# Kernel optimization log

Hardware: AMD Instinct MI355X
Metric: run time of the kernel (lower is better)

The kernel has to match this reference:

```python
import jax, jax.numpy as jnp
import numpy as np

H = 8            # n_heads
CLIP = 10.0      # tanh_clipping
CAPACITY = 1.0   # AgentVRP.VEHICLE_CAPACITY


def setup_inputs() -> dict:
    key = jax.random.key(0)
    ks = jax.random.split(key, 12)
    B, N, D = 256, 1000, 128
    s = 1.0 / np.sqrt(D)  # keep pre-tanh logits in a sane range
    return {
        "embeddings": jax.random.normal(ks[0], (B, N, D), jnp.float32),
        "mean_graph_emb": jax.random.normal(ks[1], (B, D), jnp.float32),
        "used_capacity": jax.random.uniform(ks[2], (B, 1), jnp.float32),
        "prev_node": jax.random.randint(ks[3], (B, 1), 0, N),
        "mask": jax.random.randint(ks[4], (B, 1, N), 0, 2).astype(bool),
        "wq_context": jax.random.normal(ks[5], (D, D), jnp.float32) * s,
        "wq_step_context": jax.random.normal(ks[6], (D + 1, D), jnp.float32) * s,
        "wk": jax.random.normal(ks[7], (D, D), jnp.float32) * s,
        "wk_tanh": jax.random.normal(ks[8], (D, D), jnp.float32) * s,
        "wv": jax.random.normal(ks[9], (D, D), jnp.float32) * s,
        "w_out": jax.random.normal(ks[10], (D, D), jnp.float32) * s,
    }


def reference(embeddings, mean_graph_emb, used_capacity, prev_node, mask,
              wq_context, wq_step_context, wk, wk_tanh, wv, w_out):
    B, N, D = embeddings.shape
    hd = D // H
    neg_inf = jnp.float32(-np.inf)

    # --- get_projections ---
    K = (embeddings @ wk).reshape(B, N, H, hd).transpose(0, 2, 1, 3)       # bhnd
    V = (embeddings @ wv).reshape(B, N, H, hd).transpose(0, 2, 1, 3)       # bhnd
    K_tanh = embeddings @ wk_tanh                                          # bnD
    Q_context = (mean_graph_emb @ wq_context)[:, None, :]                  # b1D

    # --- get_step_context ---
    cur = jnp.take_along_axis(embeddings, prev_node[:, :, None].astype(jnp.int32), axis=1)  # b1D
    step_ctx = jnp.concatenate([cur, CAPACITY - used_capacity[:, :, None]], axis=-1)        # b1(D+1)
    Q = Q_context + step_ctx @ wq_step_context                             # b1D
    Qh = Q.reshape(B, 1, H, hd).transpose(0, 2, 1, 3)                      # bh1d

    # --- decoder_mha (seq_len_q = 1) ---
    compat = jnp.einsum('bhqd,bhnd->bhqn', Qh, K) / jnp.sqrt(jnp.float32(hd))
    compat = jnp.where(mask[:, None, :, :], neg_inf, compat)
    attn = jax.nn.softmax(compat, axis=-1)
    out = jnp.einsum('bhqn,bhnd->bhqd', attn, V)
    mha = out.transpose(0, 2, 1, 3).reshape(B, 1, D) @ w_out               # b1D

    # --- get_log_p (single head, tanh-clipped) ---
    logits = jnp.einsum('bqD,bnD->bqn', mha, K_tanh) / jnp.sqrt(jnp.float32(D))
    logits = jnp.tanh(logits) * CLIP
    logits = jnp.where(mask, neg_inf, logits)
    log_p = jax.nn.log_softmax(logits, axis=-1)                            # b1n
    return log_p
```

## Files before the change

### kernel.cpp

```cpp
#include <hip/hip_runtime.h>
#include <hip/hip_bf16.h>
#include <math.h>

constexpr int kB = 256;
constexpr int kN = 1000;
constexpr int kD = 128;
constexpr int kH = 8;

#define MASK_FILL (-1.0e30f)

__device__ __forceinline__ bool is_masked(const void* m, int flag, int idx) {
  if (flag == 1) return ((const unsigned char*)m)[idx] != 0;
  if (flag == 0) return ((const int*)m)[idx] != 0;
  return ((const float*)m)[idx] != 0.0f;
}

__global__ __launch_bounds__(128) void q_kernel(
    const float* __restrict__ emb, const float* __restrict__ mge,
    const float* __restrict__ ucap, const int* __restrict__ prev,
    const float* __restrict__ wq_ctx, const float* __restrict__ wq_step,
    const float* __restrict__ wk, float* __restrict__ qt,
    const unsigned char* __restrict__ mb, int* __restrict__ flag) {
  const int b = blockIdx.x, t = threadIdx.x;
  __shared__ float cur[kD];
  __shared__ float Qs[kD];
  __shared__ int nonbin, off123;
  if (b == 0 && t == 0) { nonbin = 0; off123 = 0; }
  const float* crow = emb + ((size_t)b * kN + prev[b]) * kD;
  cur[t] = crow[t];
  __syncthreads();
  if (b == 0) {
    int l_nonbin = 0, l_off = 0;
    for (int i = t; i < 4096; i += 128) {
      unsigned char v = mb[i];
      if (v > 1) l_nonbin = 1;
      if (v != 0 && (i & 3) != 0) l_off = 1;
    }
    if (l_nonbin) atomicOr(&nonbin, 1);
    if (l_off) atomicOr(&off123, 1);
  }
  float acc = 0.f;
  const float* mger = mge + (size_t)b * kD;
  #pragma unroll 4
  for (int e = 0; e < kD; ++e) {
    acc += mger[e] * wq_ctx[e * kD + t];
    acc += cur[e] * wq_step[e * kD + t];
  }
  acc += (1.0f - ucap[b]) * wq_step[kD * kD + t];
  Qs[t] = acc;
  __syncthreads();
  if (b == 0 && t == 0) *flag = nonbin ? 2 : (off123 ? 1 : 0);
  float a8[8] = {};
  const float* wkrow = wk + (size_t)t * kD;
  #pragma unroll
  for (int h = 0; h < 8; ++h) {
    #pragma unroll
    for (int j = 0; j < 16; ++j)
      a8[h] += wkrow[h * 16 + j] * Qs[h * 16 + j];
  }
  #pragma unroll
  for (int h = 0; h < 8; ++h)
    qt[((size_t)b * 8 + h) * kD + t] = a8[h] * 0.25f;
}

__global__ __launch_bounds__(1024) void attn_stream_kernel(
    const float* __restrict__ emb, const float* __restrict__ qt_g,
    const void* __restrict__ mask, const int* __restrict__ flagp,
    float* __restrict__ pw, float* __restrict__ pl) {
  const int b = blockIdx.x, t = threadIdx.x;
  __shared__ __align__(16) float red[16][1024];
  __shared__ float lred[16][8];
  __shared__ unsigned char mloc[kN];
  const int flag = *flagp;
  const int sg = t & 7, hg = (t >> 3) & 3, r8 = t >> 5;
  for (int i = t; i < kN; i += 1024)
    mloc[i] = is_masked(mask, flag, b * kN + i) ? 1 : 0;
  const float* qbase = qt_g + ((size_t)b << 10) + sg * 16;
  const float* qa = qbase + (size_t)(hg * 2) * kD;
  const float* qb = qbase + (size_t)(hg * 2 + 1) * kD;
  const float4 qA0 = *reinterpret_cast<const float4*>(qa);
  const float4 qA1 = *reinterpret_cast<const float4*>(qa + 4);
  const float4 qA2 = *reinterpret_cast<const float4*>(qa + 8);
  const float4 qA3 = *reinterpret_cast<const float4*>(qa + 12);
  const float4 qB0 = *reinterpret_cast<const float4*>(qb);
  const float4 qB1 = *reinterpret_cast<const float4*>(qb + 4);
  const float4 qB2 = *reinterpret_cast<const float4*>(qb + 8);
  const float4 qB3 = *reinterpret_cast<const float4*>(qb + 12);
  float4 aA0 = {}, aA1 = {}, aA2 = {}, aA3 = {};
  float4 aB0 = {}, aB1 = {}, aB2 = {}, aB3 = {};
  float lA = 0.f, lB = 0.f;
  const float* embb = emb + (size_t)b * kN * kD + sg * 16;
  __syncthreads();
  for (int it = 0; it < 32; ++it) {
    const int n = it * 32 + r8;
    const bool valid = n < kN;
    const float* src = embb + (size_t)(valid ? n : 0) * kD;
    const float4 e0 = *reinterpret_cast<const float4*>(src);
    const float4 e1 = *reinterpret_cast<const float4*>(src + 4);
    const float4 e2 = *reinterpret_cast<const float4*>(src + 8);
    const float4 e3 = *reinterpret_cast<const float4*>(src + 12);
    float pA = e0.x*qA0.x + e0.y*qA0.y + e0.z*qA0.z + e0.w*qA0.w
             + e1.x*qA1.x + e1.y*qA1.y + e1.z*qA1.z + e1.w*qA1.w
             + e2.x*qA2.x + e2.y*qA2.y + e2.z*qA2.z + e2.w*qA2.w
             + e3.x*qA3.x + e3.y*qA3.y + e3.z*qA3.z + e3.w*qA3.w;
    float pB = e0.x*qB0.x + e0.y*qB0.y + e0.z*qB0.z + e0.w*qB0.w
             + e1.x*qB1.x + e1.y*qB1.y + e1.z*qB1.z + e1.w*qB1.w
             + e2.x*qB2.x + e2.y*qB2.y + e2.z*qB2.z + e2.w*qB2.w
             + e3.x*qB3.x + e3.y*qB3.y + e3.z*qB3.z + e3.w*qB3.w;
    pA += __shfl_xor(pA, 1, 64); pA += __shfl_xor(pA, 2, 64); pA += __shfl_xor(pA, 4, 64);
    pB += __shfl_xor(pB, 1, 64); pB += __shfl_xor(pB, 2, 64); pB += __shfl_xor(pB, 4, 64);
    const bool ok = valid && (mloc[valid ? n : 0] == 0);
    const float wA = ok ? __expf(pA) : 0.f;
    const float wB = ok ? __expf(pB) : 0.f;
    aA0.x += wA*e0.x; aA0.y += wA*e0.y; aA0.z += wA*e0.z; aA0.w += wA*e0.w;
    aA1.x += wA*e1.x; aA1.y += wA*e1.y; aA1.z += wA*e1.z; aA1.w += wA*e1.w;
    aA2.x += wA*e2.x; aA2.y += wA*e2.y; aA2.z += wA*e2.z; aA2.w += wA*e2.w;
    aA3.x += wA*e3.x; aA3.y += wA*e3.y; aA3.z += wA*e3.z; aA3.w += wA*e3.w;
    aB0.x += wB*e0.x; aB0.y += wB*e0.y; aB0.z += wB*e0.z; aB0.w += wB*e0.w;
    aB1.x += wB*e1.x; aB1.y += wB*e1.y; aB1.z += wB*e1.z; aB1.w += wB*e1.w;
    aB2.x += wB*e2.x; aB2.y += wB*e2.y; aB2.z += wB*e2.z; aB2.w += wB*e2.w;
    aB3.x += wB*e3.x; aB3.y += wB*e3.y; aB3.z += wB*e3.z; aB3.w += wB*e3.w;
    lA += wA; lB += wB;
  }
  #define M32(v) v.x += __shfl_xor(v.x,32,64); v.y += __shfl_xor(v.y,32,64); \
                 v.z += __shfl_xor(v.z,32,64); v.w += __shfl_xor(v.w,32,64);
  M32(aA0) M32(aA1) M32(aA2) M32(aA3) M32(aB0) M32(aB1) M32(aB2) M32(aB3)
  #undef M32
  lA += __shfl_xor(lA, 32, 64);
  lB += __shfl_xor(lB, 32, 64);
  const int w = t >> 6, wl = t & 63;
  if (wl < 32) {
    float* r0 = &red[w][(hg * 2) * kD + sg * 16];
    *reinterpret_cast<float4*>(r0)      = aA0;
    *reinterpret_cast<float4*>(r0 + 4)  = aA1;
    *reinterpret_cast<float4*>(r0 + 8)  = aA2;
    *reinterpret_cast<float4*>(r0 + 12) = aA3;
    float* r1 = &red[w][(hg * 2 + 1) * kD + sg * 16];
    *reinterpret_cast<float4*>(r1)      = aB0;
    *reinterpret_cast<float4*>(r1 + 4)  = aB1;
    *reinterpret_cast<float4*>(r1 + 8)  = aB2;
    *reinterpret_cast<float4*>(r1 + 12) = aB3;
    if (sg == 0) { lred[w][hg * 2] = lA; lred[w][hg * 2 + 1] = lB; }
  }
  __syncthreads();
  float v = 0.f;
  #pragma unroll
  for (int ww = 0; ww < 16; ++ww) v += red[ww][t];
  pw[((size_t)b << 10) + t] = v;
  if (t < 8) {
    float l = 0.f;
    #pragma unroll
    for (int ww = 0; ww < 16; ++ww) l += lred[ww][t];
    pl[(size_t)b * kH + t] = l;
  }
}

__global__ __launch_bounds__(1024) void logits_all_kernel(
    const float* __restrict__ emb, const void* __restrict__ mask,
    const float* __restrict__ pw, const float* __restrict__ pl,
    const float* __restrict__ wv_w, const float* __restrict__ w_out,
    const float* __restrict__ wk_tanh, float* __restrict__ out, int nsplit) {
  const int b = blockIdx.x, t = threadIdx.x;
  __shared__ float wsuml[8][132];
  __shared__ float outflat[128];
  __shared__ float mhal[128];
  __shared__ float mtl[128];
  __shared__ float linv[8];
  __shared__ float tl[kN];
  __shared__ float sums[16];
  __shared__ int nonbin_s, off_s;
  if (t == 0) { nonbin_s = 0; off_s = 0; }
  if (t < 8) {
    float l = 0.f;
    for (int s2 = 0; s2 < nsplit; ++s2)
      l += pl[(size_t)(b * nsplit + s2) * kH + t];
    linv[t] = 1.0f / l;
  }
  __syncthreads();
  {
    const unsigned char* mb = (const unsigned char*)mask;
    int ln = 0, lo = 0;
    for (int i = t; i < 4096; i += 1024) {
      const unsigned char v = mb[i];
      if (v > 1) ln = 1;
      if (v != 0 && (i & 3) != 0) lo = 1;
    }
    if (ln) atomicOr(&nonbin_s, 1);
    if (lo) atomicOr(&off_s, 1);
  }
  {
    const int h = t >> 7, d = t & 127;
    float v = 0.f;
    for (int s2 = 0; s2 < nsplit; ++s2)
      v += pw[(size_t)(b * nsplit + s2) * 1024 + t];
    wsuml[h][d] = v * linv[h];
  }
  __syncthreads();
  const int flag = nonbin_s ? 2 : (off_s ? 1 : 0);
  const int j = t >> 3, sg = t & 7;
  {
    const int h = j >> 4;
    float pp = 0.f;
    #pragma unroll
    for (int jj = 0; jj < 16; ++jj) {
      const int d = sg * 16 + jj;
      pp += wsuml[h][d] * wv_w[(size_t)d * kD + j];
    }
    pp += __shfl_xor(pp, 1, 64);
    pp += __shfl_xor(pp, 2, 64);
    pp += __shfl_xor(pp, 4, 64);
    if (sg == 0) outflat[j] = pp;
  }
  __syncthreads();
  {
    float pp = 0.f;
    #pragma unroll
    for (int jj = 0; jj < 16; ++jj) {
      const int d = sg * 16 + jj;
      pp += outflat[d] * w_out[(size_t)d * kD + j];
    }
    pp += __shfl_xor(pp, 1, 64);
    pp += __shfl_xor(pp, 2, 64);
    pp += __shfl_xor(pp, 4, 64);
    if (sg == 0) mhal[j] = pp;
  }
  __syncthreads();
  {
    float pp = 0.f;
    const float* wr = wk_tanh + (size_t)j * kD + sg * 16;
    #pragma unroll
    for (int jj = 0; jj < 16; ++jj)
      pp += wr[jj] * mhal[sg * 16 + jj];
    pp += __shfl_xor(pp, 1, 64);
    pp += __shfl_xor(pp, 2, 64);
    pp += __shfl_xor(pp, 4, 64);
    if (sg == 0) mtl[j] = pp * 0.08838834764831845f;
  }
  __syncthreads();
  const int seg = t & 7, r8 = t >> 3;
  const float* mtb = &mtl[seg * 16];
  const float4 m0 = *reinterpret_cast<const float4*>(mtb);
  const float4 m1 = *reinterpret_cast<const float4*>(mtb + 4);
  const float4 m2 = *reinterpret_cast<const float4*>(mtb + 8);
  const float4 m3 = *reinterpret_cast<const float4*>(mtb + 12);
  float sumexp = 0.f;
  const float* embb = emb + (size_t)b * kN * kD;
  #pragma unroll
  for (int it = 0; it < 8; ++it) {
    const int n = it * 128 + r8;
    const bool valid = n < kN;
    const int nc = valid ? n : kN - 1;
    const float* row = embb + (size_t)nc * kD + seg * 16;
    const float4 e0 = *reinterpret_cast<const float4*>(row);
    const float4 e1 = *reinterpret_cast<const float4*>(row + 4);
    const float4 e2 = *reinterpret_cast<const float4*>(row + 8);
    const float4 e3 = *reinterpret_cast<const float4*>(row + 12);
    float p = e0.x * m0.x + e0.y * m0.y + e0.z * m0.z + e0.w * m0.w
            + e1.x * m1.x + e1.y * m1.y + e1.z * m1.z + e1.w * m1.w
            + e2.x * m2.x + e2.y * m2.y + e2.z * m2.z + e2.w * m2.w
            + e3.x * m3.x + e3.y * m3.y + e3.z * m3.z + e3.w * m3.w;
    p += __shfl_xor(p, 1, 64);
    p += __shfl_xor(p, 2, 64);
    p += __shfl_xor(p, 4, 64);
    if (valid && seg == 0) {
      if (is_masked(mask, flag, b * kN + n)) {
        tl[n] = MASK_FILL;
      } else {
        const float tv = tanhf(p) * 10.0f;
        tl[n] = tv;
        sumexp += __expf(tv);
      }
    }
  }
  #pragma unroll
  for (int off = 1; off < 64; off <<= 1)
    sumexp += __shfl_xor(sumexp, off, 64);
  if ((t & 63) == 0) sums[t >> 6] = sumexp;
  __syncthreads();
  if (t < kN) {
    float total = 0.f;
    #pragma unroll
    for (int i = 0; i < 16; ++i) total += sums[i];
    const float lse = logf(total);
    const float v = tl[t];
    out[(size_t)b * kN + t] = (v == MASK_FILL) ? MASK_FILL : v - lse;
  }
}

extern "C" void kernel_launch(void* const* d_in, const int* in_sizes, int n_in,
                              void* d_out, int out_size, void* d_ws, size_t ws_size,
                              hipStream_t stream) {
  const float* emb     = (const float*)d_in[0];
  const float* mge     = (const float*)d_in[1];
  const float* ucap    = (const float*)d_in[2];
  const int*   prev    = (const int*)d_in[3];
  const void*  mask    = d_in[4];
  const float* wq_ctx  = (const float*)d_in[5];
  const float* wq_step = (const float*)d_in[6];
  const float* wk      = (const float*)d_in[7];
  const float* wk_tanh = (const float*)d_in[8];
  const float* wv_w    = (const float*)d_in[9];
  const float* w_out   = (const float*)d_in[10];
  float* out = (float*)d_out;

  const size_t flag_off = 0;
  const size_t qt_off   = 256;
  const size_t qt_sz    = (size_t)kB * kH * kD * 4;
  const size_t pw_off   = qt_off + qt_sz;
  const size_t pw_sz    = (size_t)kB * kH * kD * 4;

  int*   flag = (int*)((char*)d_ws + flag_off);
  float* qt   = (float*)((char*)d_ws + qt_off);
  float* pw   = (float*)((char*)d_ws + pw_off);
  float* pl   = (float*)((char*)d_ws + pw_off + pw_sz);

  hipLaunchKernelGGL(q_kernel, dim3(kB), dim3(128), 0, stream,
                     emb, mge, ucap, prev, wq_ctx, wq_step, wk, qt,
                     (const unsigned char*)mask, flag);
  hipLaunchKernelGGL(attn_stream_kernel, dim3(kB), dim3(1024), 0, stream,
                     emb, qt, mask, flag, pw, pl);
  hipLaunchKernelGGL(logits_all_kernel, dim3(kB), dim3(1024), 0, stream,
                     emb, mask, pw, pl, wv_w, w_out, wk_tanh, out, 1);
}
```

Before: 86.39 us.

## Fuse query, attention-stream and logits kernels into one per-batch kernel

Merges the three launches (query projection, attention streaming over embeddings, logits/log-softmax) into a single kernel with one 1024-thread block per batch. Intermediates (qt, pw, pl, flag) now stay in shared memory instead of going through global workspace, and the mask flag is computed per block. This removes two launch gaps and the global round trips, and a second pass over the same batch's embeddings may hit in L2. The cost is a larger shared-memory footprint per block and serialized Q computation at the start of every block.

Result: faster. 77.15 us (median of 3 runs) (-10.7%).

```diff
diff --git a/kernel.cpp b/kernel.cpp
--- a/kernel.cpp
+++ b/kernel.cpp
@@ -15,69 +15,71 @@
   return ((const float*)m)[idx] != 0.0f;
 }
 
-__global__ __launch_bounds__(128) void q_kernel(
+__global__ __launch_bounds__(1024) void fused_all_kernel(
     const float* __restrict__ emb, const float* __restrict__ mge,
     const float* __restrict__ ucap, const int* __restrict__ prev,
     const float* __restrict__ wq_ctx, const float* __restrict__ wq_step,
-    const float* __restrict__ wk, float* __restrict__ qt,
-    const unsigned char* __restrict__ mb, int* __restrict__ flag) {
-  const int b = blockIdx.x, t = threadIdx.x;
-  __shared__ float cur[kD];
-  __shared__ float Qs[kD];
-  __shared__ int nonbin, off123;
-  if (b == 0 && t == 0) { nonbin = 0; off123 = 0; }
-  const float* crow = emb + ((size_t)b * kN + prev[b]) * kD;
-  cur[t] = crow[t];
-  __syncthreads();
-  if (b == 0) {
-    int l_nonbin = 0, l_off = 0;
-    for (int i = t; i < 4096; i += 128) {
-      unsigned char v = mb[i];
-      if (v > 1) l_nonbin = 1;
-      if (v != 0 && (i & 3) != 0) l_off = 1;
-    }
-    if (l_nonbin) atomicOr(&nonbin, 1);
-    if (l_off) atomicOr(&off123, 1);
-  }
-  float acc = 0.f;
-  const float* mger = mge + (size_t)b * kD;
-  #pragma unroll 4
-  for (int e = 0; e < kD; ++e) {
-    acc += mger[e] * wq_ctx[e * kD + t];
-    acc += cur[e] * wq_step[e * kD + t];
-  }
-  acc += (1.0f - ucap[b]) * wq_step[kD * kD + t];
-  Qs[t] = acc;
-  __syncthreads();
-  if (b == 0 && t == 0) *flag = nonbin ? 2 : (off123 ? 1 : 0);
-  float a8[8] = {};
-  const float* wkrow = wk + (size_t)t * kD;
-  #pragma unroll
-  for (int h = 0; h < 8; ++h) {
-    #pragma unroll
-    for (int j = 0; j < 16; ++j)
-      a8[h] += wkrow[h * 16 + j] * Qs[h * 16 + j];
-  }
-  #pragma unroll
-  for (int h = 0; h < 8; ++h)
-    qt[((size_t)b * 8 + h) * kD + t] = a8[h] * 0.25f;
-}
-
-__global__ __launch_bounds__(1024) void attn_stream_kernel(
-    const float* __restrict__ emb, const float* __restrict__ qt_g,
-    const void* __restrict__ mask, const int* __restrict__ flagp,
-    float* __restrict__ pw, float* __restrict__ pl) {
+    const float* __restrict__ wk, const void* __restrict__ mask,
+    const float* __restrict__ wv_w, const float* __restrict__ w_out,
+    const float* __restrict__ wk_tanh, float* __restrict__ out) {
   const int b = blockIdx.x, t = threadIdx.x;
   __shared__ __align__(16) float red[16][1024];
+  __shared__ __align__(16) float qtl[8][132];
+  __shared__ float curQ[kD];
+  __shared__ float Qs[kD];
+  __shared__ float mtl[kD];
+  __shared__ float tl[kN];
   __shared__ float lred[16][8];
+  __shared__ float linv8[8];
+  __shared__ float sums[16];
   __shared__ unsigned char mloc[kN];
-  const int flag = *flagp;
-  const int sg = t & 7, hg = (t >> 3) & 3, r8 = t >> 5;
+  __shared__ int nonbin_s, off_s;
+  if (t == 0) { nonbin_s = 0; off_s = 0; }
+  if (t < kD) curQ[t] = emb[((size_t)b * kN + prev[b]) * kD + t];
+  {
+    const unsigned char* mb = (const unsigned char*)mask;
+    int ln = 0, lo = 0;
+    for (int i = t; i < 4096; i += 1024) {
+      const unsigned char v = mb[i];
+      if (v > 1) ln = 1;
+      if (v != 0 && (i & 3) != 0) lo = 1;
+    }
+    if (ln) atomicOr(&nonbin_s, 1);
+    if (lo) atomicOr(&off_s, 1);
+  }
+  __syncthreads();
+  const int flag = nonbin_s ? 2 : (off_s ? 1 : 0);
   for (int i = t; i < kN; i += 1024)
     mloc[i] = is_masked(mask, flag, b * kN + i) ? 1 : 0;
-  const float* qbase = qt_g + ((size_t)b << 10) + sg * 16;
-  const float* qa = qbase + (size_t)(hg * 2) * kD;
-  const float* qb = qbase + (size_t)(hg * 2 + 1) * kD;
+  {
+    const int j = t >> 3, sgq = t & 7;
+    float qacc = 0.f;
+    const float* mger = mge + (size_t)b * kD;
+    #pragma unroll
+    for (int jj = 0; jj < 16; ++jj) {
+      const int e = sgq * 16 + jj;
+      qacc += mger[e] * wq_ctx[(size_t)e * kD + j]
+            + curQ[e] * wq_step[(size_t)e * kD + j];
+    }
+    qacc += __shfl_xor(qacc, 1, 64);
+    qacc += __shfl_xor(qacc, 2, 64);
+    qacc += __shfl_xor(qacc, 4, 64);
+    if (sgq == 0) Qs[j] = qacc + (1.0f - ucap[b]) * wq_step[(size_t)kD * kD + j];
+  }
+  __syncthreads();
+  {
+    const int h = t >> 7, d = t & 127;
+    const float* wkr = wk + (size_t)d * kD + h * 16;
+    const float* qsr = &Qs[h * 16];
+    float a = 0.f;
+    #pragma unroll
+    for (int j = 0; j < 16; ++j) a += wkr[j] * qsr[j];
+    qtl[h][d] = a * 0.25f;
+  }
+  __syncthreads();
+  const int sg = t & 7, hg = (t >> 3) & 3, r8 = t >> 5;
+  const float* qa = &qtl[hg * 2][sg * 16];
+  const float* qb = &qtl[hg * 2 + 1][sg * 16];
   const float4 qA0 = *reinterpret_cast<const float4*>(qa);
   const float4 qA1 = *reinterpret_cast<const float4*>(qa + 4);
   const float4 qA2 = *reinterpret_cast<const float4*>(qa + 8);
@@ -90,7 +92,6 @@
   float4 aB0 = {}, aB1 = {}, aB2 = {}, aB3 = {};
   float lA = 0.f, lB = 0.f;
   const float* embb = emb + (size_t)b * kN * kD + sg * 16;
-  __syncthreads();
   for (int it = 0; it < 32; ++it) {
     const int n = it * 32 + r8;
     const bool valid = n < kN;
@@ -128,8 +129,8 @@
   #undef M32
   lA += __shfl_xor(lA, 32, 64);
   lB += __shfl_xor(lB, 32, 64);
-  const int w = t >> 6, wl = t & 63;
-  if (wl < 32) {
+  const int w = t >> 6, wlane = t & 63;
+  if (wlane < 32) {
     float* r0 = &red[w][(hg * 2) * kD + sg * 16];
     *reinterpret_cast<float4*>(r0)      = aA0;
     *reinterpret_cast<float4*>(r0 + 4)  = aA1;
@@ -143,114 +144,74 @@
     if (sg == 0) { lred[w][hg * 2] = lA; lred[w][hg * 2 + 1] = lB; }
   }
   __syncthreads();
-  float v = 0.f;
-  #pragma unroll
-  for (int ww = 0; ww < 16; ++ww) v += red[ww][t];
-  pw[((size_t)b << 10) + t] = v;
   if (t < 8) {
     float l = 0.f;
     #pragma unroll
     for (int ww = 0; ww < 16; ++ww) l += lred[ww][t];
-    pl[(size_t)b * kH + t] = l;
-  }
-}
-
-__global__ __launch_bounds__(1024) void logits_all_kernel(
-    const float* __restrict__ emb, const void* __restrict__ mask,
-    const float* __restrict__ pw, const float* __restrict__ pl,
-    const float* __restrict__ wv_w, const float* __restrict__ w_out,
-    const float* __restrict__ wk_tanh, float* __restrict__ out, int nsplit) {
-  const int b = blockIdx.x, t = threadIdx.x;
-  __shared__ float wsuml[8][132];
-  __shared__ float outflat[128];
-  __shared__ float mhal[128];
-  __shared__ float mtl[128];
-  __shared__ float linv[8];
-  __shared__ float tl[kN];
-  __shared__ float sums[16];
-  __shared__ int nonbin_s, off_s;
-  if (t == 0) { nonbin_s = 0; off_s = 0; }
-  if (t < 8) {
-    float l = 0.f;
-    for (int s2 = 0; s2 < nsplit; ++s2)
-      l += pl[(size_t)(b * nsplit + s2) * kH + t];
-    linv[t] = 1.0f / l;
-  }
-  __syncthreads();
-  {
-    const unsigned char* mb = (const unsigned char*)mask;
-    int ln = 0, lo = 0;
-    for (int i = t; i < 4096; i += 1024) {
-      const unsigned char v = mb[i];
-      if (v > 1) ln = 1;
-      if (v != 0 && (i & 3) != 0) lo = 1;
-    }
-    if (ln) atomicOr(&nonbin_s, 1);
-    if (lo) atomicOr(&off_s, 1);
-  }
-  {
-    const int h = t >> 7, d = t & 127;
+    linv8[t] = 1.0f / l;
+  }
+  __syncthreads();
+  {
     float v = 0.f;
-    for (int s2 = 0; s2 < nsplit; ++s2)
-      v += pw[(size_t)(b * nsplit + s2) * 1024 + t];
-    wsuml[h][d] = v * linv[h];
-  }
-  __syncthreads();
-  const int flag = nonbin_s ? 2 : (off_s ? 1 : 0);
-  const int j = t >> 3, sg = t & 7;
+    #pragma unroll
+    for (int ww = 0; ww < 16; ++ww) v += red[ww][t];
+    qtl[t >> 7][t & 127] = v * linv8[t >> 7];
+  }
+  __syncthreads();
+  const int j = t >> 3, sgq = t & 7;
   {
     const int h = j >> 4;
     float pp = 0.f;
     #pragma unroll
     for (int jj = 0; jj < 16; ++jj) {
-      const int d = sg * 16 + jj;
-      pp += wsuml[h][d] * wv_w[(size_t)d * kD + j];
+      const int d = sgq * 16 + jj;
+      pp += qtl[h][d] * wv_w[(size_t)d * kD + j];
     }
     pp += __shfl_xor(pp, 1, 64);
     pp += __shfl_xor(pp, 2, 64);
     pp += __shfl_xor(pp, 4, 64);
-    if (sg == 0) outflat[j] = pp;
+    if (sgq == 0) curQ[j] = pp;
   }
   __syncthreads();
   {
     float pp = 0.f;
     #pragma unroll
     for (int jj = 0; jj < 16; ++jj) {
-      const int d = sg * 16 + jj;
-      pp += outflat[d] * w_out[(size_t)d * kD + j];
+      const int d = sgq * 16 + jj;
+      pp += curQ[d] * w_out[(size_t)d * kD + j];
     }
     pp += __shfl_xor(pp, 1, 64);
     pp += __shfl_xor(pp, 2, 64);
     pp += __shfl_xor(pp, 4, 64);
-    if (sg == 0) mhal[j] = pp;
+    if (sgq == 0) Qs[j] = pp;
   }
   __syncthreads();
   {
     float pp = 0.f;
-    const float* wr = wk_tanh + (size_t)j * kD + sg * 16;
+    const float* wr = wk_tanh + (size_t)j * kD + sgq * 16;
     #pragma unroll
     for (int jj = 0; jj < 16; ++jj)
-      pp += wr[jj] * mhal[sg * 16 + jj];
+      pp += wr[jj] * Qs[sgq * 16 + jj];
     pp += __shfl_xor(pp, 1, 64);
     pp += __shfl_xor(pp, 2, 64);
     pp += __shfl_xor(pp, 4, 64);
-    if (sg == 0) mtl[j] = pp * 0.08838834764831845f;
-  }
-  __syncthreads();
-  const int seg = t & 7, r8 = t >> 3;
+    if (sgq == 0) mtl[j] = pp * 0.08838834764831845f;
+  }
+  __syncthreads();
+  const int seg = t & 7, rr8 = t >> 3;
   const float* mtb = &mtl[seg * 16];
   const float4 m0 = *reinterpret_cast<const float4*>(mtb);
   const float4 m1 = *reinterpret_cast<const float4*>(mtb + 4);
   const float4 m2 = *reinterpret_cast<const float4*>(mtb + 8);
   const float4 m3 = *reinterpret_cast<const float4*>(mtb + 12);
   float sumexp = 0.f;
-  const float* embb = emb + (size_t)b * kN * kD;
+  const float* embb2 = emb + (size_t)b * kN * kD;
   #pragma unroll
   for (int it = 0; it < 8; ++it) {
-    const int n = it * 128 + r8;
+    const int n = it * 128 + rr8;
     const bool valid = n < kN;
     const int nc = valid ? n : kN - 1;
-    const float* row = embb + (size_t)nc * kD + seg * 16;
+    const float* row = embb2 + (size_t)nc * kD + seg * 16;
     const float4 e0 = *reinterpret_cast<const float4*>(row);
     const float4 e1 = *reinterpret_cast<const float4*>(row + 4);
     const float4 e2 = *reinterpret_cast<const float4*>(row + 8);
@@ -263,7 +224,7 @@
     p += __shfl_xor(p, 2, 64);
     p += __shfl_xor(p, 4, 64);
     if (valid && seg == 0) {
-      if (is_masked(mask, flag, b * kN + n)) {
+      if (mloc[n]) {
         tl[n] = MASK_FILL;
       } else {
         const float tv = tanhf(p) * 10.0f;
@@ -303,22 +264,7 @@
   const float* w_out   = (const float*)d_in[10];
   float* out = (float*)d_out;
 
-  const size_t flag_off = 0;
-  const size_t qt_off   = 256;
-  const size_t qt_sz    = (size_t)kB * kH * kD * 4;
-  const size_t pw_off   = qt_off + qt_sz;
-  const size_t pw_sz    = (size_t)kB * kH * kD * 4;
-
-  int*   flag = (int*)((char*)d_ws + flag_off);
-  float* qt   = (float*)((char*)d_ws + qt_off);
-  float* pw   = (float*)((char*)d_ws + pw_off);
-  float* pl   = (float*)((char*)d_ws + pw_off + pw_sz);
-
-  hipLaunchKernelGGL(q_kernel, dim3(kB), dim3(128), 0, stream,
-                     emb, mge, ucap, prev, wq_ctx, wq_step, wk, qt,
-                     (const unsigned char*)mask, flag);
-  hipLaunchKernelGGL(attn_stream_kernel, dim3(kB), dim3(1024), 0, stream,
-                     emb, qt, mask, flag, pw, pl);
-  hipLaunchKernelGGL(logits_all_kernel, dim3(kB), dim3(1024), 0, stream,
-                     emb, mask, pw, pl, wv_w, w_out, wk_tanh, out, 1);
+  hipLaunchKernelGGL(fused_all_kernel, dim3(kB), dim3(1024), 0, stream,
+                     emb, mge, ucap, prev, wq_ctx, wq_step, wk, mask,
+                     wv_w, w_out, wk_tanh, out);
 }
```
